# Performance work log

Measured on AMD Instinct MI355X. Metric: run time of the kernel, lower is better.

Reference implementation:

```python
import jax, jax.numpy as jnp
import numpy as np

B, T, F_, H, HEADS = 16, 64, 64, 64, 4
D = H // HEADS            # per-head out dim (rnn_hidden // heads)
DEG = 16                  # avg degree of random feature graph
NEG_SLOPE = 0.2           # DGL GATConv default leaky_relu slope


def setup_inputs() -> dict:
    key = jax.random.key(0)
    ks = jax.random.split(key, 10)
    rng = np.random.default_rng(0)
    src_r = rng.integers(0, F_, size=F_ * DEG)
    dst_r = rng.integers(0, F_, size=F_ * DEG)
    loops = np.arange(F_)  # dgl.add_self_loop
    src = jnp.asarray(np.concatenate([src_r, loops]), jnp.int32)
    dst = jnp.asarray(np.concatenate([dst_r, loops]), jnp.int32)
    s = lambda k, shape, sc: (jax.random.normal(k, shape, jnp.float32) * sc)
    return {
        "history_stack": jax.random.normal(ks[0], (B, T, F_), jnp.float32),
        "src": src,
        "dst": dst,
        "W_enc": s(ks[1], (F_, H), 0.5),           # per-feature Linear(1, H) weights
        "b_enc": s(ks[2], (F_, H), 0.1),
        "W_gat": s(ks[3], (H, HEADS * D), 0.1),    # GATConv fc (no bias)
        "attn_l": s(ks[4], (HEADS, D), 0.1),
        "attn_r": s(ks[5], (HEADS, D), 0.1),
        "b_gat": jnp.zeros((HEADS * D,), jnp.float32),
        "W_ih": s(ks[6], (F_, 3 * H, H), 0.1),     # per-feature GRU params (r,z,n order)
        "W_hh": s(ks[7], (F_, 3 * H, H), 0.1),
        "b_ih": jnp.zeros((F_, 3 * H), jnp.float32),
        "b_hh": jnp.zeros((F_, 3 * H), jnp.float32),
        "W_dec": s(ks[8], (F_, H), 0.1),           # per-feature Linear(H, 1)
        "b_dec": s(ks[9], (F_,), 0.1),
    }


def _gat(x, src, dst, W_gat, attn_l, attn_r, b_gat):
    # x: [BT, N, H] -> [BT, N, H]; same graph replicated over leading axis.
    BT, N, _ = x.shape
    feat = (x @ W_gat).reshape(BT, N, HEADS, D)
    el = jnp.einsum('bnhd,hd->bnh', feat, attn_l)
    er = jnp.einsum('bnhd,hd->bnh', feat, attn_r)
    e = jax.nn.leaky_relu(el[:, src] + er[:, dst], NEG_SLOPE)  # [BT, E, HEADS]

    def softmax_agg(e_b, feat_b):
        m = jax.ops.segment_max(e_b, dst, num_segments=N)      # per-dst max
        ex = jnp.exp(e_b - m[dst])
        den = jax.ops.segment_sum(ex, dst, num_segments=N)
        alpha = ex / den[dst]                                   # [E, HEADS]
        msg = alpha[..., None] * feat_b[src]                    # [E, HEADS, D]
        return jax.ops.segment_sum(msg, dst, num_segments=N)   # [N, HEADS, D]

    out = jax.vmap(softmax_agg)(e, feat)
    return out.reshape(BT, N, HEADS * D) + b_gat


def _gru(x, Wih, Whh, bih, bhh):
    # x: [T, B, H]; torch GRU cell with zero initial state, gate order r,z,n.
    xW = x @ Wih.T + bih  # precompute input projections: [T, B, 3H]

    def step(h, xw):
        hW = h @ Whh.T + bhh
        xr, xz, xn = jnp.split(xw, 3, -1)
        hr, hz, hn = jnp.split(hW, 3, -1)
        r = jax.nn.sigmoid(xr + hr)
        z = jax.nn.sigmoid(xz + hz)
        n = jnp.tanh(xn + r * hn)
        h_new = (1.0 - z) * n + z * h
        return h_new, h_new

    h0 = jnp.zeros((x.shape[1], x.shape[2]), x.dtype)
    _, hs = jax.lax.scan(step, h0, xW)
    return hs  # [T, B, H]


def reference(history_stack, src, dst, W_enc, b_enc, W_gat, attn_l, attn_r,
              b_gat, W_ih, W_hh, b_ih, b_hh, W_dec, b_dec):
    Bb, Tt, Ff = history_stack.shape
    # per-feature encoders: Linear(1, H) -> [B, T, F, H]
    enc = jnp.einsum('btf,fh->btfh', history_stack, W_enc) + b_enc
    x = enc.reshape(Bb * Tt, Ff, -1)
    g = _gat(x, src, dst, W_gat, attn_l, attn_r, b_gat).reshape(Bb, Tt, Ff, -1)
    # per-feature GRUs over time: vmap over F of scan over T
    xf = jnp.transpose(g, (2, 1, 0, 3))                 # [F, T, B, H]
    hs = jax.vmap(_gru)(xf, W_ih, W_hh, b_ih, b_hh)     # [F, T, B, H]
    hiddens = jnp.transpose(hs, (2, 1, 0, 3))           # [B, T, F, H]
    # per-feature decoders: Linear(H, 1), squeezed
    ans = jnp.einsum('btfh,fh->btf', hiddens, W_dec) + b_dec
    return ans, hiddens
```

## Files before the change

kernel.cpp:

```cpp
#include <hip/hip_runtime.h>
#include <hip/hip_bf16.h>
#include <math.h>

#define Bb 16
#define Tt 64
#define Ff 64
#define MAXE 2048

typedef __fp16 h2f __attribute__((ext_vector_type(2)));
__device__ __forceinline__ h2f pkh(float a, float b) {
  return __builtin_amdgcn_cvt_pkrtz(a, b);
}

__global__ __launch_bounds__(256) void kprep(
    const int* __restrict__ src, const int* __restrict__ dst, int E,
    const float* __restrict__ W_enc, const float* __restrict__ b_enc,
    const float* __restrict__ W_gat, const float* __restrict__ attn_l,
    const float* __restrict__ attn_r, const float* __restrict__ b_gat,
    int* __restrict__ off, int* __restrict__ csr,
    float* __restrict__ A, float* __restrict__ Bc,
    float* __restrict__ aA, float* __restrict__ aB,
    float* __restrict__ rA, float* __restrict__ rB) {
  __shared__ int s_src[MAXE], s_dst[MAXE];
  __shared__ int cnt[Ff], base[Ff];
  __shared__ __align__(16) float We[64][64], Be[64][64], Wg[64][64];
  __shared__ __align__(16) float As[64][64], Bs[64][64];
  __shared__ float al_s[64], ar_s[64], bg_s[64];
  int t = threadIdx.x;

  if (blockIdx.x == 0) {
    for (int e = t; e < E; e += 256) { s_src[e] = src[e]; s_dst[e] = dst[e]; }
    if (t < Ff) cnt[t] = 0;
    __syncthreads();
    for (int e = t; e < E; e += 256) atomicAdd(&cnt[s_dst[e]], 1);
    __syncthreads();
    if (t < 64) {
      int c = cnt[t];
      int inc = c;
#pragma unroll
      for (int ofs = 1; ofs < 64; ofs <<= 1) {
        int up = __shfl_up(inc, ofs, 64);
        if (t >= ofs) inc += up;
      }
      int exc = inc - c;
      off[t] = exc;
      base[t] = exc;
      if (t == 63) off[64] = inc;
      for (int chunk = 0; chunk < E; chunk += 64) {
        int e = chunk + t;
        bool valid = e < E;
        int di = valid ? s_dst[e] : 64;
        unsigned long long m = ~0ull;
#pragma unroll
        for (int bnum = 0; bnum < 7; ++bnum) {
          unsigned long long bb = __ballot((di >> bnum) & 1);
          m &= ((di >> bnum) & 1) ? bb : ~bb;
        }
        unsigned long long below = m & ((1ull << t) - 1ull);
        int rank = __popcll(below);
        if (valid) {
          int slot = base[di] + rank;
          csr[slot] = s_src[e];
          if (below == 0ull) base[di] += __popcll(m);
        }
      }
    }
    return;
  }

  for (int i = t; i < 1024; i += 256) {
    ((float4*)We)[i] = ((const float4*)W_enc)[i];
    ((float4*)Be)[i] = ((const float4*)b_enc)[i];
    ((float4*)Wg)[i] = ((const float4*)W_gat)[i];
  }
  if (t < 64) { al_s[t] = attn_l[t]; ar_s[t] = attn_r[t]; bg_s[t] = b_gat[t]; }
  __syncthreads();
  int n = t >> 2, q = t & 3;
  float accA[16], accB[16];
#pragma unroll
  for (int j = 0; j < 16; ++j) { accA[j] = 0.f; accB[j] = 0.f; }
  for (int k = 0; k < 64; ++k) {
    float we = We[n][k], be = Be[n][k];
#pragma unroll
    for (int c = 0; c < 4; ++c) {
      float4 wg = *(const float4*)&Wg[k][q * 16 + c * 4];
      accA[c*4+0] = fmaf(we, wg.x, accA[c*4+0]); accB[c*4+0] = fmaf(be, wg.x, accB[c*4+0]);
      accA[c*4+1] = fmaf(we, wg.y, accA[c*4+1]); accB[c*4+1] = fmaf(be, wg.y, accB[c*4+1]);
      accA[c*4+2] = fmaf(we, wg.z, accA[c*4+2]); accB[c*4+2] = fmaf(be, wg.z, accB[c*4+2]);
      accA[c*4+3] = fmaf(we, wg.w, accA[c*4+3]); accB[c*4+3] = fmaf(be, wg.w, accB[c*4+3]);
    }
  }
#pragma unroll
  for (int c = 0; c < 4; ++c) {
    float4 va, vb, vbg;
    va.x = accA[c*4+0]; va.y = accA[c*4+1]; va.z = accA[c*4+2]; va.w = accA[c*4+3];
    vb.x = accB[c*4+0]; vb.y = accB[c*4+1]; vb.z = accB[c*4+2]; vb.w = accB[c*4+3];
    vbg.x = vb.x + bg_s[q*16+c*4+0]; vbg.y = vb.y + bg_s[q*16+c*4+1];
    vbg.z = vb.z + bg_s[q*16+c*4+2]; vbg.w = vb.w + bg_s[q*16+c*4+3];
    *(float4*)&As[n][q*16 + c*4] = va;
    *(float4*)&Bs[n][q*16 + c*4] = vb;
    *(float4*)&A[n*64 + q*16 + c*4] = va;
    *(float4*)&Bc[n*64 + q*16 + c*4] = vbg;
  }
  __syncthreads();
  float sa = 0.f, sb = 0.f, sra = 0.f, srb = 0.f;
#pragma unroll
  for (int j = 0; j < 16; ++j) {
    float alv = al_s[q*16 + j], arv = ar_s[q*16 + j];
    float av = As[n][q*16 + j], bv = Bs[n][q*16 + j];
    sa  = fmaf(av, alv, sa);  sb  = fmaf(bv, alv, sb);
    sra = fmaf(av, arv, sra); srb = fmaf(bv, arv, srb);
  }
  aA[t] = sa; aB[t] = sb; rA[t] = sra; rB[t] = srb;
}

__global__ __launch_bounds__(256) void k_gat(
    const float* __restrict__ hist, const float* __restrict__ Ag,
    const float* __restrict__ Bg, const float* __restrict__ aAg,
    const float* __restrict__ aBg, const float* __restrict__ rAg,
    const float* __restrict__ rBg, const int* __restrict__ off,
    const int* __restrict__ csr, int E, float* __restrict__ g_out) {
  __shared__ __align__(16) float feat[64 * 68];
  __shared__ float x_s[64];
  __shared__ float el_s[64][4], er_s[64][4];
  __shared__ int csr_s[1152];
  __shared__ int off_s[Ff + 1];
  int bt = blockIdx.x, t = threadIdx.x;
  if (t < 64) x_s[t] = hist[bt * 64 + t];
  if (t < Ff + 1) off_s[t] = off[t];
  for (int e = t; e < E; e += 256) csr_s[e] = csr[e];
  __syncthreads();

  int s0 = t >> 2, q = t & 3;
  {
    float xs = x_s[s0];
    const float4* Ar = (const float4*)(Ag + (s0 << 6) + (q << 4));
    const float4* Br = (const float4*)(Bg + (s0 << 6) + (q << 4));
#pragma unroll
    for (int c = 0; c < 4; ++c) {
      float4 a4 = Ar[c], b4 = Br[c];
      float4 o;
      o.x = fmaf(xs, a4.x, b4.x); o.y = fmaf(xs, a4.y, b4.y);
      o.z = fmaf(xs, a4.z, b4.z); o.w = fmaf(xs, a4.w, b4.w);
      *(float4*)&feat[s0 * 68 + (q << 4) + (c << 2)] = o;
    }
    el_s[s0][q] = fmaf(xs, aAg[t], aBg[t]);
    er_s[s0][q] = fmaf(xs, rAg[t], rBg[t]);
  }
  __syncthreads();

  int d = s0, hd = q;
  int o0 = off_s[d], o1 = off_s[d + 1];
  float erd = er_s[d][hd];
  float den = 0.f;
  float acc[16];
#pragma unroll
  for (int j = 0; j < 16; ++j) acc[j] = 0.f;
  for (int e = o0; e < o1; ++e) {
    int s = csr_s[e];
    float ee = el_s[s][hd] + erd;
    ee = fmaxf(ee, 0.2f * ee);
    float p = __expf(ee);
    den += p;
    const float* fr = &feat[s * 68 + (hd << 4)];
#pragma unroll
    for (int c = 0; c < 4; ++c) {
      float4 fv = *(const float4*)&fr[c << 2];
      acc[c*4+0] = fmaf(p, fv.x, acc[c*4+0]);
      acc[c*4+1] = fmaf(p, fv.y, acc[c*4+1]);
      acc[c*4+2] = fmaf(p, fv.z, acc[c*4+2]);
      acc[c*4+3] = fmaf(p, fv.w, acc[c*4+3]);
    }
  }
  float inv = __builtin_amdgcn_rcpf(den);
  float* gp = g_out + (size_t)bt * 4096 + (d << 6) + (hd << 4);
#pragma unroll
  for (int c = 0; c < 4; ++c) {
    float4 o;
    o.x = acc[c*4+0] * inv; o.y = acc[c*4+1] * inv;
    o.z = acc[c*4+2] * inv; o.w = acc[c*4+3] * inv;
    *(float4*)&gp[c << 2] = o;
  }
}

__global__ __launch_bounds__(64, 1) void k_gru(
    const float* __restrict__ W_ih, const float* __restrict__ W_hh,
    const float* __restrict__ b_ih, const float* __restrict__ b_hh,
    const float* __restrict__ W_dec, const float* __restrict__ b_dec,
    float* __restrict__ hid, float* __restrict__ ans) {
  __shared__ __align__(16) h2f gall[64][32];
  __shared__ __align__(16) __fp16 h16[64];
  int blk = blockIdx.x;
  int f = blk & 63, b = blk >> 6;
  int t = threadIdx.x;

  const float* WiB = W_ih + f * 12288 + (t << 6);
  const float* WhB = W_hh + f * 12288 + (t << 6);
  h2f wi0[32], wi1[32], wi2[32], wh0[32], wh1[32], wh2[32];
#pragma unroll
  for (int c = 0; c < 16; ++c) {
    float4 v;
    v = *(const float4*)(WiB + (c << 2));
    wi0[c*2] = pkh(v.x, v.y); wi0[c*2+1] = pkh(v.z, v.w);
    v = *(const float4*)(WiB + 4096 + (c << 2));
    wi1[c*2] = pkh(v.x, v.y); wi1[c*2+1] = pkh(v.z, v.w);
    v = *(const float4*)(WiB + 8192 + (c << 2));
    wi2[c*2] = pkh(v.x, v.y); wi2[c*2+1] = pkh(v.z, v.w);
    v = *(const float4*)(WhB + (c << 2));
    wh0[c*2] = pkh(v.x, v.y); wh0[c*2+1] = pkh(v.z, v.w);
    v = *(const float4*)(WhB + 4096 + (c << 2));
    wh1[c*2] = pkh(v.x, v.y); wh1[c*2+1] = pkh(v.z, v.w);
    v = *(const float4*)(WhB + 8192 + (c << 2));
    wh2[c*2] = pkh(v.x, v.y); wh2[c*2+1] = pkh(v.z, v.w);
  }
#pragma unroll
  for (int j = 0; j < 32; ++j) {
    asm volatile("" : "+v"(wi0[j]), "+v"(wi1[j]), "+v"(wi2[j]),
                      "+v"(wh0[j]), "+v"(wh1[j]), "+v"(wh2[j]));
  }
  float bR  = b_ih[f*192 + t]       + b_hh[f*192 + t];
  float bZ  = b_ih[f*192 + 64 + t]  + b_hh[f*192 + 64 + t];
  float bXN = b_ih[f*192 + 128 + t];
  float bHN = b_hh[f*192 + 128 + t];
  float wd   = W_dec[(f << 6) + t];
  float bdec = b_dec[f];
  size_t base = (size_t)b * 262144 + (f << 6);

#pragma unroll
  for (int c = 0; c < 16; ++c) {
    float4 v = *(const float4*)&hid[base + (size_t)t * 4096 + (c << 2)];
    gall[t][c*2]     = pkh(v.x, v.y);
    gall[t][c*2+1]   = pkh(v.z, v.w);
  }
  h16[t] = (__fp16)0.f;
  __syncthreads();

  float hreg = 0.f;
#pragma unroll 1
  for (int ts = 0; ts < 64; ++ts) {
    h2f gv[32], hv[32];
#pragma unroll
    for (int j = 0; j < 8; ++j) {
      *(float4*)&gv[j*4] = *(const float4*)&gall[ts][j*4];
      *(float4*)&hv[j*4] = *(const float4*)&h16[j*8];
    }
    float p0 = 0.f, p1 = 0.f, p2 = 0.f, q0 = 0.f, q1 = 0.f, q2 = 0.f;
#pragma unroll
    for (int j = 0; j < 32; ++j) {
      p0 = __builtin_amdgcn_fdot2(gv[j], wi0[j], p0, false);
      q0 = __builtin_amdgcn_fdot2(hv[j], wh0[j], q0, false);
      p1 = __builtin_amdgcn_fdot2(gv[j], wi1[j], p1, false);
      q1 = __builtin_amdgcn_fdot2(hv[j], wh1[j], q1, false);
      p2 = __builtin_amdgcn_fdot2(gv[j], wi2[j], p2, false);
      q2 = __builtin_amdgcn_fdot2(hv[j], wh2[j], q2, false);
    }
    float rr = __builtin_amdgcn_rcpf(1.f + __expf(-(p0 + q0 + bR)));
    float zz = __builtin_amdgcn_rcpf(1.f + __expf(-(p1 + q1 + bZ)));
    float pre = fmaf(rr, q2 + bHN, p2 + bXN);
    float nn = 1.f - 2.f * __builtin_amdgcn_rcpf(1.f + __expf(2.f * pre));
    float hnew = fmaf(zz, hreg - nn, nn);
    hreg = hnew;
    h16[t] = (__fp16)hnew;
    hid[base + (size_t)ts * 4096 + t] = hnew;
    float part = hnew * wd;
    part += __shfl_xor(part, 1);
    part += __shfl_xor(part, 2);
    part += __shfl_xor(part, 4);
    part += __shfl_xor(part, 8);
    part += __shfl_xor(part, 16);
    part += __shfl_xor(part, 32);
    if (t == 0) ans[(((b << 6) + ts) << 6) + f] = part + bdec;
  }
}

extern "C" void kernel_launch(void* const* d_in, const int* in_sizes, int n_in,
                              void* d_out, int out_size, void* d_ws, size_t ws_size,
                              hipStream_t stream) {
  const float* hist   = (const float*)d_in[0];
  const int* src      = (const int*)d_in[1];
  const int* dst      = (const int*)d_in[2];
  const float* W_enc  = (const float*)d_in[3];
  const float* b_enc  = (const float*)d_in[4];
  const float* W_gat  = (const float*)d_in[5];
  const float* attn_l = (const float*)d_in[6];
  const float* attn_r = (const float*)d_in[7];
  const float* b_gat  = (const float*)d_in[8];
  const float* W_ih   = (const float*)d_in[9];
  const float* W_hh   = (const float*)d_in[10];
  const float* b_ih   = (const float*)d_in[11];
  const float* b_hh   = (const float*)d_in[12];
  const float* W_dec  = (const float*)d_in[13];
  const float* b_dec  = (const float*)d_in[14];
  int E = in_sizes[1];

  float* ans = (float*)d_out;
  float* hid = (float*)d_out + Bb * Tt * Ff;

  int* off   = (int*)d_ws;
  int* csr   = off + 256;
  float* A   = (float*)(csr + 2048);
  float* Bc  = A + 4096;
  float* aA  = Bc + 4096;
  float* aB  = aA + 256;
  float* rA  = aB + 256;
  float* rB  = rA + 256;

  hipLaunchKernelGGL(kprep, dim3(2), dim3(256), 0, stream,
                     src, dst, E, W_enc, b_enc, W_gat, attn_l, attn_r, b_gat,
                     off, csr, A, Bc, aA, aB, rA, rB);
  hipLaunchKernelGGL(k_gat, dim3(Bb * Tt), dim3(256), 0, stream,
                     hist, A, Bc, aA, aB, rA, rB, off, csr, E, hid);
  hipLaunchKernelGGL(k_gru, dim3(Ff * Bb), dim3(64), 0, stream,
                     W_ih, W_hh, b_ih, b_hh, W_dec, b_dec, hid, ans);
}
```

Baseline: 94.02 us.

## Precompute GRU input projections for all timesteps before the recurrent loop

Splits the GRU kernel into two phases. The first computes the input-to-hidden dot products for all 64 timesteps with W_ih held in registers and stores them as fp16 in shared memory. The second reloads the same registers with W_hh and runs the serial recurrence using only the hidden-state dot products. This halves the work on the sequential critical path and halves live weight registers, at the cost of extra LDS and an added fp16 rounding of the input projections.

```diff
diff --git a/kernel.cpp b/kernel.cpp
--- a/kernel.cpp
+++ b/kernel.cpp
@@ -189,34 +189,69 @@
     const float* __restrict__ W_dec, const float* __restrict__ b_dec,
     float* __restrict__ hid, float* __restrict__ ans) {
   __shared__ __align__(16) h2f gall[64][32];
+  __shared__ __fp16 xwr[64][64];
+  __shared__ __fp16 xwz[64][64];
+  __shared__ __fp16 xwn[64][64];
   __shared__ __align__(16) __fp16 h16[64];
   int blk = blockIdx.x;
   int f = blk & 63, b = blk >> 6;
   int t = threadIdx.x;
 
-  const float* WiB = W_ih + f * 12288 + (t << 6);
-  const float* WhB = W_hh + f * 12288 + (t << 6);
-  h2f wi0[32], wi1[32], wi2[32], wh0[32], wh1[32], wh2[32];
+  size_t base = (size_t)b * 262144 + (f << 6);
+
 #pragma unroll
   for (int c = 0; c < 16; ++c) {
-    float4 v;
-    v = *(const float4*)(WiB + (c << 2));
-    wi0[c*2] = pkh(v.x, v.y); wi0[c*2+1] = pkh(v.z, v.w);
-    v = *(const float4*)(WiB + 4096 + (c << 2));
-    wi1[c*2] = pkh(v.x, v.y); wi1[c*2+1] = pkh(v.z, v.w);
-    v = *(const float4*)(WiB + 8192 + (c << 2));
-    wi2[c*2] = pkh(v.x, v.y); wi2[c*2+1] = pkh(v.z, v.w);
-    v = *(const float4*)(WhB + (c << 2));
-    wh0[c*2] = pkh(v.x, v.y); wh0[c*2+1] = pkh(v.z, v.w);
-    v = *(const float4*)(WhB + 4096 + (c << 2));
-    wh1[c*2] = pkh(v.x, v.y); wh1[c*2+1] = pkh(v.z, v.w);
-    v = *(const float4*)(WhB + 8192 + (c << 2));
-    wh2[c*2] = pkh(v.x, v.y); wh2[c*2+1] = pkh(v.z, v.w);
-  }
-#pragma unroll
-  for (int j = 0; j < 32; ++j) {
-    asm volatile("" : "+v"(wi0[j]), "+v"(wi1[j]), "+v"(wi2[j]),
-                      "+v"(wh0[j]), "+v"(wh1[j]), "+v"(wh2[j]));
+    float4 v = *(const float4*)&hid[base + (size_t)t * 4096 + (c << 2)];
+    gall[t][c*2]   = pkh(v.x, v.y);
+    gall[t][c*2+1] = pkh(v.z, v.w);
+  }
+
+  h2f w0[32], w1[32], w2[32];
+  {
+    const float* WiB = W_ih + f * 12288 + (t << 6);
+#pragma unroll
+    for (int c = 0; c < 16; ++c) {
+      float4 v;
+      v = *(const float4*)(WiB + (c << 2));
+      w0[c*2] = pkh(v.x, v.y); w0[c*2+1] = pkh(v.z, v.w);
+      v = *(const float4*)(WiB + 4096 + (c << 2));
+      w1[c*2] = pkh(v.x, v.y); w1[c*2+1] = pkh(v.z, v.w);
+      v = *(const float4*)(WiB + 8192 + (c << 2));
+      w2[c*2] = pkh(v.x, v.y); w2[c*2+1] = pkh(v.z, v.w);
+    }
+  }
+  __syncthreads();
+
+#pragma unroll 1
+  for (int ts = 0; ts < 64; ++ts) {
+    h2f gv[32];
+#pragma unroll
+    for (int j = 0; j < 8; ++j)
+      *(float4*)&gv[j*4] = *(const float4*)&gall[ts][j*4];
+    float p0 = 0.f, p1 = 0.f, p2 = 0.f;
+#pragma unroll
+    for (int j = 0; j < 32; ++j) {
+      p0 = __builtin_amdgcn_fdot2(gv[j], w0[j], p0, false);
+      p1 = __builtin_amdgcn_fdot2(gv[j], w1[j], p1, false);
+      p2 = __builtin_amdgcn_fdot2(gv[j], w2[j], p2, false);
+    }
+    xwr[ts][t] = (__fp16)p0;
+    xwz[ts][t] = (__fp16)p1;
+    xwn[ts][t] = (__fp16)p2;
+  }
+
+  {
+    const float* WhB = W_hh + f * 12288 + (t << 6);
+#pragma unroll
+    for (int c = 0; c < 16; ++c) {
+      float4 v;
+      v = *(const float4*)(WhB + (c << 2));
+      w0[c*2] = pkh(v.x, v.y); w0[c*2+1] = pkh(v.z, v.w);
+      v = *(const float4*)(WhB + 4096 + (c << 2));
+      w1[c*2] = pkh(v.x, v.y); w1[c*2+1] = pkh(v.z, v.w);
+      v = *(const float4*)(WhB + 8192 + (c << 2));
+      w2[c*2] = pkh(v.x, v.y); w2[c*2+1] = pkh(v.z, v.w);
+    }
   }
   float bR  = b_ih[f*192 + t]       + b_hh[f*192 + t];
   float bZ  = b_ih[f*192 + 64 + t]  + b_hh[f*192 + 64 + t];
@@ -224,39 +259,29 @@
   float bHN = b_hh[f*192 + 128 + t];
   float wd   = W_dec[(f << 6) + t];
   float bdec = b_dec[f];
-  size_t base = (size_t)b * 262144 + (f << 6);
-
-#pragma unroll
-  for (int c = 0; c < 16; ++c) {
-    float4 v = *(const float4*)&hid[base + (size_t)t * 4096 + (c << 2)];
-    gall[t][c*2]     = pkh(v.x, v.y);
-    gall[t][c*2+1]   = pkh(v.z, v.w);
-  }
   h16[t] = (__fp16)0.f;
   __syncthreads();
 
   float hreg = 0.f;
 #pragma unroll 1
   for (int ts = 0; ts < 64; ++ts) {
-    h2f gv[32], hv[32];
-#pragma unroll
-    for (int j = 0; j < 8; ++j) {
-      *(float4*)&gv[j*4] = *(const float4*)&gall[ts][j*4];
+    float xr = (float)xwr[ts][t];
+    float xz = (float)xwz[ts][t];
+    float xn = (float)xwn[ts][t];
+    h2f hv[32];
+#pragma unroll
+    for (int j = 0; j < 8; ++j)
       *(float4*)&hv[j*4] = *(const float4*)&h16[j*8];
-    }
-    float p0 = 0.f, p1 = 0.f, p2 = 0.f, q0 = 0.f, q1 = 0.f, q2 = 0.f;
+    float q0 = 0.f, q1 = 0.f, q2 = 0.f;
 #pragma unroll
     for (int j = 0; j < 32; ++j) {
-      p0 = __builtin_amdgcn_fdot2(gv[j], wi0[j], p0, false);
-      q0 = __builtin_amdgcn_fdot2(hv[j], wh0[j], q0, false);
-      p1 = __builtin_amdgcn_fdot2(gv[j], wi1[j], p1, false);
-      q1 = __builtin_amdgcn_fdot2(hv[j], wh1[j], q1, false);
-      p2 = __builtin_amdgcn_fdot2(gv[j], wi2[j], p2, false);
-      q2 = __builtin_amdgcn_fdot2(hv[j], wh2[j], q2, false);
-    }
-    float rr = __builtin_amdgcn_rcpf(1.f + __expf(-(p0 + q0 + bR)));
-    float zz = __builtin_amdgcn_rcpf(1.f + __expf(-(p1 + q1 + bZ)));
-    float pre = fmaf(rr, q2 + bHN, p2 + bXN);
+      q0 = __builtin_amdgcn_fdot2(hv[j], w0[j], q0, false);
+      q1 = __builtin_amdgcn_fdot2(hv[j], w1[j], q1, false);
+      q2 = __builtin_amdgcn_fdot2(hv[j], w2[j], q2, false);
+    }
+    float rr = __builtin_amdgcn_rcpf(1.f + __expf(-(q0 + xr + bR)));
+    float zz = __builtin_amdgcn_rcpf(1.f + __expf(-(q1 + xz + bZ)));
+    float pre = fmaf(rr, q2 + bHN, xn + bXN);
     float nn = 1.f - 2.f * __builtin_amdgcn_rcpf(1.f + __expf(2.f * pre));
     float hnew = fmaf(zz, hreg - nn, nn);
     hreg = hnew;
```

New measurement: 93.44 us. Within noise of the previous version (-0.6%).
